# Performance work log

Hardware: AMD Instinct MI355X
Metric: run time of the kernel (lower is better)

The kernel has to match this reference:

```python
import jax, jax.numpy as jnp
import numpy as np

N = 50000       # n_nodes
E = 800000      # n_edges
DIN = 64
DH = 64
DOUT = 64


def setup_inputs() -> dict:
    key = jax.random.key(0)
    k0, k1, k2, k3, k4 = jax.random.split(key, 5)
    x = jax.random.normal(k0, (N, DIN), dtype=jnp.float32)
    edge_index = jax.random.randint(k1, (2, E), 0, N, dtype=jnp.int32)
    # learnable per-edge weight (nn.Parameter); positive init keeps gcn_norm well-defined
    edge_weight = jax.random.uniform(k2, (E,), jnp.float32, 0.1, 1.0)
    W1 = jax.random.normal(k3, (DH, DIN), dtype=jnp.float32) * (1.0 / np.sqrt(DIN))
    b1 = jnp.zeros((DH,), jnp.float32)
    W2 = jax.random.normal(k4, (DOUT, DH), dtype=jnp.float32) * (1.0 / np.sqrt(DH))
    b2 = jnp.zeros((DOUT,), jnp.float32)
    return {"x": x, "edge_weight": edge_weight, "W1": W1, "b1": b1,
            "W2": W2, "b2": b2, "edge_index": edge_index}


def _gcn_norm(edge_index, edge_weight, n):
    # PyG gcn_norm: add self-loops (weight 1), symmetric normalization.
    loop = jnp.arange(n, dtype=edge_index.dtype)
    row = jnp.concatenate([edge_index[0], loop])   # source nodes
    col = jnp.concatenate([edge_index[1], loop])   # target nodes
    w = jnp.concatenate([edge_weight, jnp.ones((n,), edge_weight.dtype)])
    deg = jax.ops.segment_sum(w, col, num_segments=n)
    dinv = jnp.where(deg > 0, jax.lax.rsqrt(jnp.where(deg > 0, deg, 1.0)), 0.0)
    norm = dinv[row] * w * dinv[col]               # [E + N]
    return row, col, norm


def _gcn_layer(x, W, b, row, col, norm, n):
    h = x @ W.T                                     # [N, out]
    # gather source features, scale by norm, scatter-add into targets
    out = jax.ops.segment_sum(h[row] * norm[:, None], col, num_segments=n)
    return out + b


def reference(x, edge_weight, W1, b1, W2, b2, edge_index):
    n = x.shape[0]
    row, col, norm = _gcn_norm(edge_index, edge_weight, n)
    h = _gcn_layer(x, W1, b1, row, col, norm, n)
    h = jax.nn.relu(h)                              # self.pre: ReLU + Dropout (identity in eval)
    return _gcn_layer(h, W2, b2, row, col, norm, n)
```

## Files before the change

kernel.cpp:

```cpp
#include <hip/hip_runtime.h>

#define D 64
#define GN 128
#define SW 68
#define SX 132
#define MAXDEG 64
#define RBITS_C 8
#define RANGE_C 256
#define MAXB_C 5120
#define RANGE_F 64
#define APB 2048
#define AGW 8

typedef unsigned long long u64;
typedef unsigned int u32;
typedef unsigned short u16;
typedef unsigned char u8;

__device__ __forceinline__ float4 fma4(float4 w, float s, float4 c) {
    c.x = fmaf(w.x, s, c.x); c.y = fmaf(w.y, s, c.y);
    c.z = fmaf(w.z, s, c.z); c.w = fmaf(w.w, s, c.w);
    return c;
}

__device__ __forceinline__ u32 f2bf(float f) {
    u32 u = __float_as_uint(f);
    return (u + 0x7FFFu + ((u >> 16) & 1u)) >> 16;
}
__device__ __forceinline__ u32 pack2(float a, float b) { return f2bf(a) | (f2bf(b) << 16); }
__device__ __forceinline__ float blo(u32 u) { return __uint_as_float(u << 16); }
__device__ __forceinline__ float bhi(u32 u) { return __uint_as_float(u & 0xFFFF0000u); }

__global__ __launch_bounds__(256) void k_bucket(
        const int* __restrict__ ei, const float* __restrict__ ew,
        u64* __restrict__ barr, u32* __restrict__ gcount, int E, int NB) {
    __shared__ u64 srec[APB];
    __shared__ u8  sbkt[APB];
    __shared__ u32 scnt[256];
    __shared__ u32 sbase[256];

    int t = threadIdx.x;
    int e0 = blockIdx.x * APB;
    int ne = min(APB, E - e0);

    for (int i = t; i < 256; i += 256) scnt[i] = 0;
    __syncthreads();

    for (int i = t; i < ne; i += 256) {
        int e   = e0 + i;
        int r   = ei[e];
        int c   = ei[(size_t)E + e];
        float w = ew[e];
        int b   = c >> RBITS_C;
        srec[i] = ((u64)__float_as_uint(w) << 32)
                | (u32)r | ((u32)(c & (RANGE_C - 1)) << 20);
        sbkt[i] = (u8)b;
        atomicAdd(&scnt[b], 1u);
    }
    __syncthreads();

    for (int i = t; i < NB; i += 256) {
        u32 cnt = scnt[i];
        sbase[i] = cnt ? atomicAdd(&gcount[i], cnt) : 0u;
        scnt[i] = 0;
    }
    __syncthreads();

    for (int i = t; i < ne; i += 256) {
        int b   = sbkt[i];
        u32 rk  = atomicAdd(&scnt[b], 1u);
        u32 pos = sbase[b] + rk;
        if (pos < MAXB_C) barr[(size_t)b * MAXB_C + pos] = srec[i];
    }
}

__global__ __launch_bounds__(256) void k_csr(
        const u64* __restrict__ barr, const u32* __restrict__ gcount,
        u64* __restrict__ degcnt, int2* __restrict__ eg, int N) {
    __shared__ __align__(16) int2 seg[RANGE_F * MAXDEG];
    __shared__ u32   scnt[RANGE_F];
    __shared__ float sdeg[RANGE_F];

    int fb = blockIdx.x;
    int cb = fb >> 2;
    int sub = fb & 3;
    int t = threadIdx.x;
    u32 cnt = min(gcount[cb], (u32)MAXB_C);
    int base_c = fb << 6;

    if (t < RANGE_F) { scnt[t] = 0; sdeg[t] = 1.0f; }
    int4* sz = (int4*)seg;
    for (int i = t; i < RANGE_F * MAXDEG / 2; i += 256) sz[i] = make_int4(0, 0, 0, 0);
    __syncthreads();

    const u64* bp = barr + (size_t)cb * MAXB_C;
    for (u32 i = t; i < cnt; i += 256) {
        u64 rec = bp[i];
        int cl8 = (int)((rec >> 20) & 0xFFu);
        if ((cl8 >> 6) != sub) continue;
        int cl  = cl8 & (RANGE_F - 1);
        int src = (int)(rec & 0xFFFFFu);
        u32 wb  = (u32)(rec >> 32);
        u32 rank = atomicAdd(&scnt[cl], 1u);
        atomicAdd(&sdeg[cl], __uint_as_float(wb));
        if (rank < MAXDEG) seg[(cl << 6) + rank] = make_int2(src, (int)wb);
    }
    __syncthreads();

    if (t < RANGE_F) {
        int n = base_c + t;
        if (n < N) {
            u32 c2 = min(scnt[t], (u32)MAXDEG);
            float dd = rsqrtf(sdeg[t]);
            degcnt[n] = ((u64)c2 << 32) | (u64)__float_as_uint(dd);
        }
    }

    int nt = min(RANGE_F, N - base_c);
    const int4* s4 = (const int4*)seg;
    int4* d4 = (int4*)(eg + ((size_t)base_c << 6));
    int tot = nt << 5;
    for (int i = t; i < tot; i += 256) d4[i] = s4[i];
}

__global__ __launch_bounds__(256) void k_gemm(
        const float* __restrict__ in, const float* __restrict__ W,
        u16* __restrict__ h, int N) {
    __shared__ __align__(16) float sWt[D * SW];
    __shared__ __align__(16) float sxT[D * SX];

    int t = threadIdx.x;
    int node0 = blockIdx.x * GN;

    for (int i = t; i < D * D / 4; i += 256) {
        int j = i >> 4, k4 = i & 15;
        float4 w = ((const float4*)W)[i];
        sWt[(4 * k4 + 0) * SW + j] = w.x;
        sWt[(4 * k4 + 1) * SW + j] = w.y;
        sWt[(4 * k4 + 2) * SW + j] = w.z;
        sWt[(4 * k4 + 3) * SW + j] = w.w;
    }
    for (int i = t; i < GN * D / 4; i += 256) {
        int nn = i >> 4, k4 = i & 15;
        int n = node0 + nn;
        float4 v = make_float4(0.f, 0.f, 0.f, 0.f);
        if (n < N) v = ((const float4*)(in + (size_t)n * D))[k4];
        sxT[(4 * k4 + 0) * SX + nn] = v.x;
        sxT[(4 * k4 + 1) * SX + nn] = v.y;
        sxT[(4 * k4 + 2) * SX + nn] = v.z;
        sxT[(4 * k4 + 3) * SX + nn] = v.w;
    }
    __syncthreads();

    int jg = (t & 7) * 8;
    int ng = (t >> 3) * 4;
    float4 a0[4], a1[4];
    #pragma unroll
    for (int a = 0; a < 4; ++a) {
        a0[a] = make_float4(0.f, 0.f, 0.f, 0.f);
        a1[a] = make_float4(0.f, 0.f, 0.f, 0.f);
    }

    #pragma unroll 8
    for (int k = 0; k < D; ++k) {
        const float* wr = &sWt[k * SW + jg];
        float4 w0 = *(const float4*)wr;
        float4 w1 = *(const float4*)(wr + 4);
        float4 xv = *(const float4*)&sxT[k * SX + ng];
        a0[0] = fma4(w0, xv.x, a0[0]);  a1[0] = fma4(w1, xv.x, a1[0]);
        a0[1] = fma4(w0, xv.y, a0[1]);  a1[1] = fma4(w1, xv.y, a1[1]);
        a0[2] = fma4(w0, xv.z, a0[2]);  a1[2] = fma4(w1, xv.z, a1[2]);
        a0[3] = fma4(w0, xv.w, a0[3]);  a1[3] = fma4(w1, xv.w, a1[3]);
    }

    #pragma unroll
    for (int a = 0; a < 4; ++a) {
        int n = node0 + ng + a;
        if (n >= N) continue;
        uint4 st;
        st.x = pack2(a0[a].x, a0[a].y);
        st.y = pack2(a0[a].z, a0[a].w);
        st.z = pack2(a1[a].x, a1[a].y);
        st.w = pack2(a1[a].z, a1[a].w);
        *(uint4*)(h + (size_t)n * D + jg) = st;
    }
}

__device__ __forceinline__ void gather8(
        const u16* __restrict__ h, const u32* __restrict__ dv,
        const int2* __restrict__ eg, const float* __restrict__ bias,
        u64* __restrict__ sedge,
        int n, int lane, float acc[8]) {
    int g = lane >> 3;
    int f = (lane & 7) * 8;
    u64 dcn = ((const u64*)dv)[n];
    int c = min((int)(dcn >> 32), MAXDEG);
    float dinv_n = __uint_as_float((u32)dcn);

    size_t s = (size_t)n << 6;
    int2 ee = eg[s + lane];
    float di = __uint_as_float(dv[(size_t)ee.x << 1]);
    float wf = __int_as_float(ee.y) * di * dinv_n;
    sedge[lane] = ((u64)__float_as_uint(wf) << 32) | (u32)ee.x;

    #pragma unroll
    for (int i = 0; i < 8; ++i) acc[i] = 0.f;

    if (g == 0) {
        float d2 = dinv_n * dinv_n;
        uint4 hv = *(const uint4*)(h + ((size_t)n << 6) + f);
        float4 b0 = *(const float4*)(bias + f);
        float4 b1 = *(const float4*)(bias + f + 4);
        acc[0] = fmaf(blo(hv.x), d2, b0.x); acc[1] = fmaf(bhi(hv.x), d2, b0.y);
        acc[2] = fmaf(blo(hv.y), d2, b0.z); acc[3] = fmaf(bhi(hv.y), d2, b0.w);
        acc[4] = fmaf(blo(hv.z), d2, b1.x); acc[5] = fmaf(bhi(hv.z), d2, b1.y);
        acc[6] = fmaf(blo(hv.w), d2, b1.z); acc[7] = fmaf(bhi(hv.w), d2, b1.w);
    }

    #pragma unroll
    for (int k = 0; k < 8; ++k) {
        int e = g + (k << 3);
        if (e < c) {
            u64 rec = sedge[e];
            int src = (int)(u32)rec;
            float w = __uint_as_float((u32)(rec >> 32));
            uint4 hv = *(const uint4*)(h + ((size_t)src << 6) + f);
            acc[0] = fmaf(blo(hv.x), w, acc[0]); acc[1] = fmaf(bhi(hv.x), w, acc[1]);
            acc[2] = fmaf(blo(hv.y), w, acc[2]); acc[3] = fmaf(bhi(hv.y), w, acc[3]);
            acc[4] = fmaf(blo(hv.z), w, acc[4]); acc[5] = fmaf(bhi(hv.z), w, acc[5]);
            acc[6] = fmaf(blo(hv.w), w, acc[6]); acc[7] = fmaf(bhi(hv.w), w, acc[7]);
        }
    }
}

__global__ __launch_bounds__(512) void k_agg_g2(
        const u16* __restrict__ h, const u64* __restrict__ degcnt,
        const int2* __restrict__ eg, const float* __restrict__ b1,
        const float* __restrict__ W2, u16* __restrict__ h2, int N) {
    __shared__ __align__(16) float4 sA[8 * 64];
    __shared__ __align__(16) float4 sB[8 * 64];
    __shared__ u64 sedge[AGW][64];

    int t = threadIdx.x;
    {
        int jj = t >> 6, l = t & 63;
        int gg = l >> 3, kk = l & 7;
        const float4* w4 = (const float4*)(W2 + ((size_t)(gg * 8 + jj) << 6) + kk * 8);
        sA[t] = w4[0];
        sB[t] = w4[1];
    }
    __syncthreads();

    int wid = t >> 6;
    int n = blockIdx.x * AGW + wid;
    if (n >= N) return;
    int lane = t & 63;

    float acc[8];
    gather8(h, (const u32*)degcnt, eg, b1, sedge[wid], n, lane, acc);

    #pragma unroll
    for (int k = 0; k < 8; ++k) {
        acc[k] += __shfl_xor(acc[k], 8);
        acc[k] += __shfl_xor(acc[k], 16);
        acc[k] += __shfl_xor(acc[k], 32);
    }

    float r[8];
    #pragma unroll
    for (int k = 0; k < 8; ++k) r[k] = fmaxf(acc[k], 0.f);

    int g = lane >> 3;
    float p[8];
    #pragma unroll
    for (int jj = 0; jj < 8; ++jj) {
        float4 wa = sA[(jj << 6) + lane];
        float4 wb = sB[(jj << 6) + lane];
        float v;
        v = r[0] * wa.x;         v = fmaf(r[1], wa.y, v);
        v = fmaf(r[2], wa.z, v); v = fmaf(r[3], wa.w, v);
        v = fmaf(r[4], wb.x, v); v = fmaf(r[5], wb.y, v);
        v = fmaf(r[6], wb.z, v); v = fmaf(r[7], wb.w, v);
        p[jj] = v;
    }
    #pragma unroll
    for (int jj = 0; jj < 8; ++jj) {
        p[jj] += __shfl_xor(p[jj], 1);
        p[jj] += __shfl_xor(p[jj], 2);
        p[jj] += __shfl_xor(p[jj], 4);
    }

    if ((lane & 7) == 0) {
        uint4 st;
        st.x = pack2(p[0], p[1]);
        st.y = pack2(p[2], p[3]);
        st.z = pack2(p[4], p[5]);
        st.w = pack2(p[6], p[7]);
        *(uint4*)(h2 + ((size_t)n << 6) + g * 8) = st;
    }
}

__global__ __launch_bounds__(256) void k_aggregate(
        const u16* __restrict__ h, const u64* __restrict__ degcnt,
        const int2* __restrict__ eg, const float* __restrict__ b,
        float* __restrict__ out, int N) {
    __shared__ u64 sedge[4][64];

    int t = threadIdx.x;
    int wid = t >> 6;
    int n = blockIdx.x * 4 + wid;
    if (n >= N) return;
    int lane = t & 63;

    float acc[8];
    gather8(h, (const u32*)degcnt, eg, b, sedge[wid], n, lane, acc);

    #pragma unroll
    for (int k = 0; k < 8; ++k) {
        acc[k] += __shfl_xor(acc[k], 8);
        acc[k] += __shfl_xor(acc[k], 16);
        acc[k] += __shfl_xor(acc[k], 32);
    }

    if ((lane >> 3) == 0) {
        int f = (lane & 7) * 8;
        float4* o = (float4*)(out + ((size_t)n << 6) + f);
        o[0] = make_float4(acc[0], acc[1], acc[2], acc[3]);
        o[1] = make_float4(acc[4], acc[5], acc[6], acc[7]);
    }
}

extern "C" void kernel_launch(void* const* d_in, const int* in_sizes, int n_in,
                              void* d_out, int out_size, void* d_ws, size_t ws_size,
                              hipStream_t stream) {
    const float* x  = (const float*)d_in[0];
    const float* ew = (const float*)d_in[1];
    const float* W1 = (const float*)d_in[2];
    const float* b1 = (const float*)d_in[3];
    const float* W2 = (const float*)d_in[4];
    const float* b2 = (const float*)d_in[5];
    const int*   ei = (const int*)d_in[6];

    int N = in_sizes[0] / D;
    int E = in_sizes[1];
    int NBC = (N + RANGE_C - 1) >> RBITS_C;
    int NBF = (N + RANGE_F - 1) / RANGE_F;
    float* out = (float*)d_out;

    char* p = (char*)d_ws;
    u64*   degcnt = (u64*)p;   p += (size_t)N * 8;
    int2*  eg     = (int2*)p;  p += (size_t)N * MAXDEG * 8;
    u16*   h      = (u16*)p;   p += (size_t)N * D * 2;
    u16*   h2     = (u16*)p;   p += (size_t)N * D * 2;
    u64*   barr   = (u64*)p;   p += (size_t)NBC * MAXB_C * 8;
    u32*   gcount = (u32*)p;   p += 4096;

    dim3 blk(256);
    int gemm_grid   = (N + GN - 1) / GN;
    int bucket_grid = (E + APB - 1) / APB;
    int aggf_grid   = (N + AGW - 1) / AGW;
    int agg_grid    = (N + 3) / 4;

    hipMemsetAsync(gcount, 0, 4096, stream);

    k_bucket<<<dim3(bucket_grid), blk, 0, stream>>>(ei, ew, barr, gcount, E, NBC);
    k_csr<<<dim3(NBF), blk, 0, stream>>>(barr, gcount, degcnt, eg, N);

    k_gemm<<<dim3(gemm_grid), blk, 0, stream>>>(x, W1, h, N);

    k_agg_g2<<<dim3(aggf_grid), dim3(512), 0, stream>>>(h, degcnt, eg, b1, W2, h2, N);

    k_aggregate<<<dim3(agg_grid), blk, 0, stream>>>(h2, degcnt, eg, b2, out, N);
}
```

Measured before the change: 185.7 us.

## Process several nodes per wave with prefetch and cache edge norms between layers

Each wavefront in both aggregation kernels now handles four consecutive nodes, prefetching the next node's edge list and self-features while gathering the current one. The first aggregation writes the computed per-edge normalized weight back into the edge array, so the second aggregation skips the random dinv lookup. The CSR build no longer zeroes shared memory and copies only the valid edge slots to global memory. Fewer waves means less latency hiding through parallelism, and the in-place edge rewrite adds a dependency between the two kernels.

```diff
diff --git a/kernel.cpp b/kernel.cpp
--- a/kernel.cpp
+++ b/kernel.cpp
@@ -10,7 +10,7 @@
 #define MAXB_C 5120
 #define RANGE_F 64
 #define APB 2048
-#define AGW 8
+#define NPW 4
 
 typedef unsigned long long u64;
 typedef unsigned int u32;
@@ -89,8 +89,6 @@
     int base_c = fb << 6;
 
     if (t < RANGE_F) { scnt[t] = 0; sdeg[t] = 1.0f; }
-    int4* sz = (int4*)seg;
-    for (int i = t; i < RANGE_F * MAXDEG / 2; i += 256) sz[i] = make_int4(0, 0, 0, 0);
     __syncthreads();
 
     const u64* bp = barr + (size_t)cb * MAXB_C;
@@ -120,7 +118,11 @@
     const int4* s4 = (const int4*)seg;
     int4* d4 = (int4*)(eg + ((size_t)base_c << 6));
     int tot = nt << 5;
-    for (int i = t; i < tot; i += 256) d4[i] = s4[i];
+    for (int i = t; i < tot; i += 256) {
+        int cl = i >> 5;
+        int lv = (int)min(scnt[cl], (u32)MAXDEG);
+        if (((i & 31) << 1) < lv) d4[i] = s4[i];
+    }
 }
 
 __global__ __launch_bounds__(256) void k_gemm(
@@ -186,42 +188,26 @@
     }
 }
 
-__device__ __forceinline__ void gather8(
-        const u16* __restrict__ h, const u32* __restrict__ dv,
-        const int2* __restrict__ eg, const float* __restrict__ bias,
-        u64* __restrict__ sedge,
-        int n, int lane, float acc[8]) {
-    int g = lane >> 3;
-    int f = (lane & 7) * 8;
-    u64 dcn = ((const u64*)dv)[n];
-    int c = min((int)(dcn >> 32), MAXDEG);
-    float dinv_n = __uint_as_float((u32)dcn);
-
-    size_t s = (size_t)n << 6;
-    int2 ee = eg[s + lane];
-    float di = __uint_as_float(dv[(size_t)ee.x << 1]);
-    float wf = __int_as_float(ee.y) * di * dinv_n;
-    sedge[lane] = ((u64)__float_as_uint(wf) << 32) | (u32)ee.x;
-
-    #pragma unroll
-    for (int i = 0; i < 8; ++i) acc[i] = 0.f;
+__device__ __forceinline__ void gather_core(
+        const u16* __restrict__ h, const u64* __restrict__ se,
+        int c, int g, int f, float dinv_n, uint4 selfh,
+        float4 bia, float4 bib, float acc[8]) {
+    #pragma unroll
+    for (int q = 0; q < 8; ++q) acc[q] = 0.f;
 
     if (g == 0) {
         float d2 = dinv_n * dinv_n;
-        uint4 hv = *(const uint4*)(h + ((size_t)n << 6) + f);
-        float4 b0 = *(const float4*)(bias + f);
-        float4 b1 = *(const float4*)(bias + f + 4);
-        acc[0] = fmaf(blo(hv.x), d2, b0.x); acc[1] = fmaf(bhi(hv.x), d2, b0.y);
-        acc[2] = fmaf(blo(hv.y), d2, b0.z); acc[3] = fmaf(bhi(hv.y), d2, b0.w);
-        acc[4] = fmaf(blo(hv.z), d2, b1.x); acc[5] = fmaf(bhi(hv.z), d2, b1.y);
-        acc[6] = fmaf(blo(hv.w), d2, b1.z); acc[7] = fmaf(bhi(hv.w), d2, b1.w);
+        acc[0] = fmaf(blo(selfh.x), d2, bia.x); acc[1] = fmaf(bhi(selfh.x), d2, bia.y);
+        acc[2] = fmaf(blo(selfh.y), d2, bia.z); acc[3] = fmaf(bhi(selfh.y), d2, bia.w);
+        acc[4] = fmaf(blo(selfh.z), d2, bib.x); acc[5] = fmaf(bhi(selfh.z), d2, bib.y);
+        acc[6] = fmaf(blo(selfh.w), d2, bib.z); acc[7] = fmaf(bhi(selfh.w), d2, bib.w);
     }
 
     #pragma unroll
     for (int k = 0; k < 8; ++k) {
         int e = g + (k << 3);
         if (e < c) {
-            u64 rec = sedge[e];
+            u64 rec = se[e];
             int src = (int)(u32)rec;
             float w = __uint_as_float((u32)(rec >> 32));
             uint4 hv = *(const uint4*)(h + ((size_t)src << 6) + f);
@@ -235,11 +221,11 @@
 
 __global__ __launch_bounds__(512) void k_agg_g2(
         const u16* __restrict__ h, const u64* __restrict__ degcnt,
-        const int2* __restrict__ eg, const float* __restrict__ b1,
+        int2* __restrict__ eg, const float* __restrict__ b1,
         const float* __restrict__ W2, u16* __restrict__ h2, int N) {
     __shared__ __align__(16) float4 sA[8 * 64];
     __shared__ __align__(16) float4 sB[8 * 64];
-    __shared__ u64 sedge[AGW][64];
+    __shared__ u64 sedge[8][64];
 
     int t = threadIdx.x;
     {
@@ -251,52 +237,96 @@
     }
     __syncthreads();
 
-    int wid = t >> 6;
-    int n = blockIdx.x * AGW + wid;
-    if (n >= N) return;
-    int lane = t & 63;
-
-    float acc[8];
-    gather8(h, (const u32*)degcnt, eg, b1, sedge[wid], n, lane, acc);
-
-    #pragma unroll
-    for (int k = 0; k < 8; ++k) {
-        acc[k] += __shfl_xor(acc[k], 8);
-        acc[k] += __shfl_xor(acc[k], 16);
-        acc[k] += __shfl_xor(acc[k], 32);
-    }
-
-    float r[8];
-    #pragma unroll
-    for (int k = 0; k < 8; ++k) r[k] = fmaxf(acc[k], 0.f);
-
-    int g = lane >> 3;
-    float p[8];
-    #pragma unroll
-    for (int jj = 0; jj < 8; ++jj) {
-        float4 wa = sA[(jj << 6) + lane];
-        float4 wb = sB[(jj << 6) + lane];
-        float v;
-        v = r[0] * wa.x;         v = fmaf(r[1], wa.y, v);
-        v = fmaf(r[2], wa.z, v); v = fmaf(r[3], wa.w, v);
-        v = fmaf(r[4], wb.x, v); v = fmaf(r[5], wb.y, v);
-        v = fmaf(r[6], wb.z, v); v = fmaf(r[7], wb.w, v);
-        p[jj] = v;
-    }
-    #pragma unroll
-    for (int jj = 0; jj < 8; ++jj) {
-        p[jj] += __shfl_xor(p[jj], 1);
-        p[jj] += __shfl_xor(p[jj], 2);
-        p[jj] += __shfl_xor(p[jj], 4);
-    }
-
-    if ((lane & 7) == 0) {
-        uint4 st;
-        st.x = pack2(p[0], p[1]);
-        st.y = pack2(p[2], p[3]);
-        st.z = pack2(p[4], p[5]);
-        st.w = pack2(p[6], p[7]);
-        *(uint4*)(h2 + ((size_t)n << 6) + g * 8) = st;
+    int wid = t >> 6, lane = t & 63;
+    int g = lane >> 3, f = (lane & 7) * 8;
+    u64* se = sedge[wid];
+    const u32* dv = (const u32*)degcnt;
+    int base = (blockIdx.x * 8 + wid) * NPW;
+    if (base >= N) return;
+
+    float4 bia = *(const float4*)(b1 + f);
+    float4 bib = *(const float4*)(b1 + f + 4);
+
+    u64 dcn[NPW];
+    #pragma unroll
+    for (int i = 0; i < NPW; ++i) {
+        int n = base + i;
+        dcn[i] = (n < N) ? degcnt[n] : 0;
+    }
+
+    int2 ee_nxt = make_int2(0, 0);
+    uint4 sh_nxt = make_uint4(0, 0, 0, 0);
+    {
+        int c0 = min((int)(dcn[0] >> 32), MAXDEG);
+        if (lane < c0) ee_nxt = eg[((size_t)base << 6) + lane];
+        if (g == 0) sh_nxt = *(const uint4*)(h + ((size_t)base << 6) + f);
+    }
+
+    #pragma unroll
+    for (int i = 0; i < NPW; ++i) {
+        int n = base + i;
+        int c = min((int)(dcn[i] >> 32), MAXDEG);
+        float dinv_n = __uint_as_float((u32)dcn[i]);
+        int2 ee = ee_nxt;
+        uint4 selfh = sh_nxt;
+
+        if (lane < c) {
+            float di = __uint_as_float(dv[(size_t)ee.x << 1]);
+            float wf = __int_as_float(ee.y) * di * dinv_n;
+            eg[((size_t)n << 6) + lane] = make_int2(ee.x, __float_as_int(wf));
+            se[lane] = ((u64)__float_as_uint(wf) << 32) | (u32)ee.x;
+        }
+
+        if (i < NPW - 1) {
+            int n1 = base + i + 1;
+            int c1 = min((int)(dcn[i + 1] >> 32), MAXDEG);
+            if (lane < c1) ee_nxt = eg[((size_t)n1 << 6) + lane];
+            if (g == 0 && n1 < N) sh_nxt = *(const uint4*)(h + ((size_t)n1 << 6) + f);
+        }
+
+        if (n >= N) continue;
+
+        float acc[8];
+        gather_core(h, se, c, g, f, dinv_n, selfh, bia, bib, acc);
+
+        #pragma unroll
+        for (int k = 0; k < 8; ++k) {
+            acc[k] += __shfl_xor(acc[k], 8);
+            acc[k] += __shfl_xor(acc[k], 16);
+            acc[k] += __shfl_xor(acc[k], 32);
+        }
+
+        float r[8];
+        #pragma unroll
+        for (int k = 0; k < 8; ++k) r[k] = fmaxf(acc[k], 0.f);
+
+        float p[8];
+        #pragma unroll
+        for (int jj = 0; jj < 8; ++jj) {
+            float4 wa = sA[(jj << 6) + lane];
+            float4 wb = sB[(jj << 6) + lane];
+            float v;
+            v = r[0] * wa.x;         v = fmaf(r[1], wa.y, v);
+            v = fmaf(r[2], wa.z, v); v = fmaf(r[3], wa.w, v);
+            v = fmaf(r[4], wb.x, v); v = fmaf(r[5], wb.y, v);
+            v = fmaf(r[6], wb.z, v); v = fmaf(r[7], wb.w, v);
+            p[jj] = v;
+        }
+        #pragma unroll
+        for (int jj = 0; jj < 8; ++jj) {
+            p[jj] += __shfl_xor(p[jj], 1);
+            p[jj] += __shfl_xor(p[jj], 2);
+            p[jj] += __shfl_xor(p[jj], 4);
+        }
+
+        if ((lane & 7) == 0) {
+            uint4 st;
+            st.x = pack2(p[0], p[1]);
+            st.y = pack2(p[2], p[3]);
+            st.z = pack2(p[4], p[5]);
+            st.w = pack2(p[6], p[7]);
+            *(uint4*)(h2 + ((size_t)n << 6) + g * 8) = st;
+        }
     }
 }
 
@@ -306,27 +336,65 @@
         float* __restrict__ out, int N) {
     __shared__ u64 sedge[4][64];
 
-    int t = threadIdx.x;
-    int wid = t >> 6;
-    int n = blockIdx.x * 4 + wid;
-    if (n >= N) return;
-    int lane = t & 63;
-
-    float acc[8];
-    gather8(h, (const u32*)degcnt, eg, b, sedge[wid], n, lane, acc);
-
-    #pragma unroll
-    for (int k = 0; k < 8; ++k) {
-        acc[k] += __shfl_xor(acc[k], 8);
-        acc[k] += __shfl_xor(acc[k], 16);
-        acc[k] += __shfl_xor(acc[k], 32);
-    }
-
-    if ((lane >> 3) == 0) {
-        int f = (lane & 7) * 8;
-        float4* o = (float4*)(out + ((size_t)n << 6) + f);
-        o[0] = make_float4(acc[0], acc[1], acc[2], acc[3]);
-        o[1] = make_float4(acc[4], acc[5], acc[6], acc[7]);
+    int t = threadIdx.x, wid = t >> 6, lane = t & 63;
+    int g = lane >> 3, f = (lane & 7) * 8;
+    u64* se = sedge[wid];
+    int base = (blockIdx.x * 4 + wid) * NPW;
+    if (base >= N) return;
+
+    float4 bia = *(const float4*)(b + f);
+    float4 bib = *(const float4*)(b + f + 4);
+
+    u64 dcn[NPW];
+    #pragma unroll
+    for (int i = 0; i < NPW; ++i) {
+        int n = base + i;
+        dcn[i] = (n < N) ? degcnt[n] : 0;
+    }
+
+    int2 ee_nxt = make_int2(0, 0);
+    uint4 sh_nxt = make_uint4(0, 0, 0, 0);
+    {
+        int c0 = min((int)(dcn[0] >> 32), MAXDEG);
+        if (lane < c0) ee_nxt = eg[((size_t)base << 6) + lane];
+        if (g == 0) sh_nxt = *(const uint4*)(h + ((size_t)base << 6) + f);
+    }
+
+    #pragma unroll
+    for (int i = 0; i < NPW; ++i) {
+        int n = base + i;
+        int c = min((int)(dcn[i] >> 32), MAXDEG);
+        float dinv_n = __uint_as_float((u32)dcn[i]);
+        int2 ee = ee_nxt;
+        uint4 selfh = sh_nxt;
+
+        if (lane < c)
+            se[lane] = ((u64)(u32)ee.y << 32) | (u32)ee.x;
+
+        if (i < NPW - 1) {
+            int n1 = base + i + 1;
+            int c1 = min((int)(dcn[i + 1] >> 32), MAXDEG);
+            if (lane < c1) ee_nxt = eg[((size_t)n1 << 6) + lane];
+            if (g == 0 && n1 < N) sh_nxt = *(const uint4*)(h + ((size_t)n1 << 6) + f);
+        }
+
+        if (n >= N) continue;
+
+        float acc[8];
+        gather_core(h, se, c, g, f, dinv_n, selfh, bia, bib, acc);
+
+        #pragma unroll
+        for (int k = 0; k < 8; ++k) {
+            acc[k] += __shfl_xor(acc[k], 8);
+            acc[k] += __shfl_xor(acc[k], 16);
+            acc[k] += __shfl_xor(acc[k], 32);
+        }
+
+        if (g == 0) {
+            float4* o = (float4*)(out + ((size_t)n << 6) + f);
+            o[0] = make_float4(acc[0], acc[1], acc[2], acc[3]);
+            o[1] = make_float4(acc[4], acc[5], acc[6], acc[7]);
+        }
     }
 }
 
@@ -358,8 +426,8 @@
     dim3 blk(256);
     int gemm_grid   = (N + GN - 1) / GN;
     int bucket_grid = (E + APB - 1) / APB;
-    int aggf_grid   = (N + AGW - 1) / AGW;
-    int agg_grid    = (N + 3) / 4;
+    int aggf_grid   = (N + 8 * NPW - 1) / (8 * NPW);
+    int agg_grid    = (N + 4 * NPW - 1) / (4 * NPW);
 
     hipMemsetAsync(gcount, 0, 4096, stream);
 
```

Result: slower. 197.1 us (+6.2%).

## Precompute normalized edge weights once and copy only valid CSR slots

Applied to the files above, without the earlier changes.

Adds a k_fold kernel that rewrites each padded CSR slot's weight to the full symmetric norm (w * dinv[src] * dinv[dst]) once, so both aggregation kernels no longer do the dependent dinv[src] gather per edge. Both aggregation passes now load edge records only for lanes below the node's degree. The CSR build skips zeroing shared memory and writes only the valid prefix of each node's 64-slot segment, cutting global writes. The cost is an extra kernel launch plus a read-modify-write pass over the edge array.

```diff
diff --git a/kernel.cpp b/kernel.cpp
--- a/kernel.cpp
+++ b/kernel.cpp
@@ -10,7 +10,6 @@
 #define MAXB_C 5120
 #define RANGE_F 64
 #define APB 2048
-#define AGW 8
 
 typedef unsigned long long u64;
 typedef unsigned int u32;
@@ -89,8 +88,6 @@
     int base_c = fb << 6;
 
     if (t < RANGE_F) { scnt[t] = 0; sdeg[t] = 1.0f; }
-    int4* sz = (int4*)seg;
-    for (int i = t; i < RANGE_F * MAXDEG / 2; i += 256) sz[i] = make_int4(0, 0, 0, 0);
     __syncthreads();
 
     const u64* bp = barr + (size_t)cb * MAXB_C;
@@ -120,7 +117,31 @@
     const int4* s4 = (const int4*)seg;
     int4* d4 = (int4*)(eg + ((size_t)base_c << 6));
     int tot = nt << 5;
-    for (int i = t; i < tot; i += 256) d4[i] = s4[i];
+    for (int i = t; i < tot; i += 256) {
+        int cl = i >> 5;
+        int lv = (int)min(scnt[cl], (u32)MAXDEG);
+        if (((i & 31) << 1) < lv) d4[i] = s4[i];
+    }
+}
+
+__global__ __launch_bounds__(256) void k_fold(
+        const u64* __restrict__ degcnt, int2* __restrict__ eg, int N, int nwaves) {
+    int lane = threadIdx.x & 63;
+    int w0 = blockIdx.x * 4 + (threadIdx.x >> 6);
+    const u32* dv = (const u32*)degcnt;
+
+    for (int n = w0; n < N; n += nwaves) {
+        u64 dcn = degcnt[n];
+        int c = min((int)(dcn >> 32), MAXDEG);
+        float dinv_n = __uint_as_float((u32)dcn);
+        if (lane < c) {
+            size_t s = ((size_t)n << 6) + lane;
+            int2 ee = eg[s];
+            float di = __uint_as_float(dv[(size_t)ee.x << 1]);
+            float wf = __int_as_float(ee.y) * di * dinv_n;
+            eg[s] = make_int2(ee.x, __float_as_int(wf));
+        }
+    }
 }
 
 __global__ __launch_bounds__(256) void k_gemm(
@@ -187,21 +208,21 @@
 }
 
 __device__ __forceinline__ void gather8(
-        const u16* __restrict__ h, const u32* __restrict__ dv,
-        const int2* __restrict__ eg, const float* __restrict__ bias,
-        u64* __restrict__ sedge,
+        const u16* __restrict__ h, const u64* __restrict__ degcnt,
+        const int2* __restrict__ eg, float4 bia, float4 bib,
+        u64* __restrict__ se,
         int n, int lane, float acc[8]) {
     int g = lane >> 3;
     int f = (lane & 7) * 8;
-    u64 dcn = ((const u64*)dv)[n];
+    u64 dcn = degcnt[n];
     int c = min((int)(dcn >> 32), MAXDEG);
     float dinv_n = __uint_as_float((u32)dcn);
 
     size_t s = (size_t)n << 6;
-    int2 ee = eg[s + lane];
-    float di = __uint_as_float(dv[(size_t)ee.x << 1]);
-    float wf = __int_as_float(ee.y) * di * dinv_n;
-    sedge[lane] = ((u64)__float_as_uint(wf) << 32) | (u32)ee.x;
+    if (lane < c) {
+        int2 ee = eg[s + lane];
+        se[lane] = ((u64)(u32)ee.y << 32) | (u32)ee.x;
+    }
 
     #pragma unroll
     for (int i = 0; i < 8; ++i) acc[i] = 0.f;
@@ -209,19 +230,17 @@
     if (g == 0) {
         float d2 = dinv_n * dinv_n;
         uint4 hv = *(const uint4*)(h + ((size_t)n << 6) + f);
-        float4 b0 = *(const float4*)(bias + f);
-        float4 b1 = *(const float4*)(bias + f + 4);
-        acc[0] = fmaf(blo(hv.x), d2, b0.x); acc[1] = fmaf(bhi(hv.x), d2, b0.y);
-        acc[2] = fmaf(blo(hv.y), d2, b0.z); acc[3] = fmaf(bhi(hv.y), d2, b0.w);
-        acc[4] = fmaf(blo(hv.z), d2, b1.x); acc[5] = fmaf(bhi(hv.z), d2, b1.y);
-        acc[6] = fmaf(blo(hv.w), d2, b1.z); acc[7] = fmaf(bhi(hv.w), d2, b1.w);
+        acc[0] = fmaf(blo(hv.x), d2, bia.x); acc[1] = fmaf(bhi(hv.x), d2, bia.y);
+        acc[2] = fmaf(blo(hv.y), d2, bia.z); acc[3] = fmaf(bhi(hv.y), d2, bia.w);
+        acc[4] = fmaf(blo(hv.z), d2, bib.x); acc[5] = fmaf(bhi(hv.z), d2, bib.y);
+        acc[6] = fmaf(blo(hv.w), d2, bib.z); acc[7] = fmaf(bhi(hv.w), d2, bib.w);
     }
 
     #pragma unroll
     for (int k = 0; k < 8; ++k) {
         int e = g + (k << 3);
         if (e < c) {
-            u64 rec = sedge[e];
+            u64 rec = se[e];
             int src = (int)(u32)rec;
             float w = __uint_as_float((u32)(rec >> 32));
             uint4 hv = *(const uint4*)(h + ((size_t)src << 6) + f);
@@ -239,7 +258,7 @@
         const float* __restrict__ W2, u16* __restrict__ h2, int N) {
     __shared__ __align__(16) float4 sA[8 * 64];
     __shared__ __align__(16) float4 sB[8 * 64];
-    __shared__ u64 sedge[AGW][64];
+    __shared__ u64 sedge[8][64];
 
     int t = threadIdx.x;
     {
@@ -251,13 +270,16 @@
     }
     __syncthreads();
 
-    int wid = t >> 6;
-    int n = blockIdx.x * AGW + wid;
+    int wid = t >> 6, lane = t & 63;
+    int n = blockIdx.x * 8 + wid;
     if (n >= N) return;
-    int lane = t & 63;
+    int g = lane >> 3, f = (lane & 7) * 8;
+
+    float4 bia = *(const float4*)(b1 + f);
+    float4 bib = *(const float4*)(b1 + f + 4);
 
     float acc[8];
-    gather8(h, (const u32*)degcnt, eg, b1, sedge[wid], n, lane, acc);
+    gather8(h, degcnt, eg, bia, bib, sedge[wid], n, lane, acc);
 
     #pragma unroll
     for (int k = 0; k < 8; ++k) {
@@ -270,7 +292,6 @@
     #pragma unroll
     for (int k = 0; k < 8; ++k) r[k] = fmaxf(acc[k], 0.f);
 
-    int g = lane >> 3;
     float p[8];
     #pragma unroll
     for (int jj = 0; jj < 8; ++jj) {
@@ -306,14 +327,16 @@
         float* __restrict__ out, int N) {
     __shared__ u64 sedge[4][64];
 
-    int t = threadIdx.x;
-    int wid = t >> 6;
+    int t = threadIdx.x, wid = t >> 6, lane = t & 63;
     int n = blockIdx.x * 4 + wid;
     if (n >= N) return;
-    int lane = t & 63;
+    int g = lane >> 3, f = (lane & 7) * 8;
+
+    float4 bia = *(const float4*)(b + f);
+    float4 bib = *(const float4*)(b + f + 4);
 
     float acc[8];
-    gather8(h, (const u32*)degcnt, eg, b, sedge[wid], n, lane, acc);
+    gather8(h, degcnt, eg, bia, bib, sedge[wid], n, lane, acc);
 
     #pragma unroll
     for (int k = 0; k < 8; ++k) {
@@ -322,8 +345,7 @@
         acc[k] += __shfl_xor(acc[k], 32);
     }
 
-    if ((lane >> 3) == 0) {
-        int f = (lane & 7) * 8;
+    if (g == 0) {
         float4* o = (float4*)(out + ((size_t)n << 6) + f);
         o[0] = make_float4(acc[0], acc[1], acc[2], acc[3]);
         o[1] = make_float4(acc[4], acc[5], acc[6], acc[7]);
@@ -358,13 +380,15 @@
     dim3 blk(256);
     int gemm_grid   = (N + GN - 1) / GN;
     int bucket_grid = (E + APB - 1) / APB;
-    int aggf_grid   = (N + AGW - 1) / AGW;
+    int fold_grid   = 3125;
+    int aggf_grid   = (N + 7) / 8;
     int agg_grid    = (N + 3) / 4;
 
     hipMemsetAsync(gcount, 0, 4096, stream);
 
     k_bucket<<<dim3(bucket_grid), blk, 0, stream>>>(ei, ew, barr, gcount, E, NBC);
     k_csr<<<dim3(NBF), blk, 0, stream>>>(barr, gcount, degcnt, eg, N);
+    k_fold<<<dim3(fold_grid), blk, 0, stream>>>(degcnt, eg, N, fold_grid * 4);
 
     k_gemm<<<dim3(gemm_grid), blk, 0, stream>>>(x, W1, h, N);
 
```

Result: slower. 193.4 us (+4.1%).
